# Performance work log

Hardware: AMD Instinct MI355X
Metric: run time of the kernel (lower is better)

## Reference

```python
import jax, jax.numpy as jnp
import numpy as np

B = 8192
D_LS, D_A, D_LM, D_AT, D_DS, D_DM = 1024, 512, 512, 512, 1024, 512
LENGTH = D_LS + D_A + D_LM  # 2048
OUT = 512


def setup_inputs() -> dict:
    key = jax.random.key(0)
    ks = jax.random.split(key, 9)
    return {
        "result_ls": jax.random.normal(ks[0], (B, 1, D_LS), jnp.float32),
        "result_A": jax.random.normal(ks[1], (B, 1, D_A), jnp.float32),
        "result_lm": jax.random.normal(ks[2], (B, 1, D_LM), jnp.float32),
        "result_AT": jax.random.normal(ks[3], (B, 1, D_AT), jnp.float32),
        "result_ds": jax.random.normal(ks[4], (B, 1, D_DS), jnp.float32),
        "result_dm": jax.random.normal(ks[5], (B, 1, D_DM), jnp.float32),
        "W": jax.random.normal(ks[6], (OUT, LENGTH), jnp.float32) * (1.0 / np.sqrt(LENGTH)),
        "b": jax.random.normal(ks[7], (OUT,), jnp.float32) * 0.01,
        "h_n": jax.random.normal(ks[8], (OUT, 1), jnp.float32) * (1.0 / np.sqrt(OUT)),
    }


def _pad_to(x, length):
    # zero-pad last dim of [B,1,d] to [B,1,length]
    return jnp.pad(x, ((0, 0), (0, 0), (0, length - x.shape[2])))


def reference(result_ls, result_A, result_lm, result_AT, result_ds, result_dm, W, b, h_n):
    # pad each node-type feature to common length and stack along node axis -> [B,6,L]
    nodes = jnp.concatenate(
        [_pad_to(t, LENGTH) for t in (result_ls, result_A, result_lm, result_AT, result_ds, result_dm)],
        axis=1,
    )
    temp = jnp.tanh(jnp.einsum("bnl,ol->bno", nodes, W) + b)  # [B,6,OUT]
    score = jnp.einsum("bno,oi->bni", temp, h_n)               # [B,6,1]
    score = score.reshape(-1, 1, 6)
    beta = jax.nn.softmax(score, axis=2)                        # [B,1,6]
    z_i = jnp.matmul(beta, nodes)                               # [B,1,L]
    return z_i
```

## Files before the change

kernel.cpp:

```cpp
#include <hip/hip_runtime.h>
#include <hip/hip_bf16.h>
#include <stdint.h>

typedef __attribute__((ext_vector_type(8))) short bf16x8;
typedef __attribute__((ext_vector_type(4))) float f32x4;

#define NB 8192

__device__ __forceinline__ unsigned pkbf(float x, float y) {
    __hip_bfloat162 h = __float22bfloat162_rn(make_float2(x, y));
    unsigned r;
    __builtin_memcpy(&r, &h, 4);
    return r;
}

__device__ __forceinline__ uint4 pack8(float4 a, float4 b) {
    uint4 r;
    r.x = pkbf(a.x, a.y);
    r.y = pkbf(a.z, a.w);
    r.z = pkbf(b.x, b.y);
    r.w = pkbf(b.z, b.w);
    return r;
}

__global__ __launch_bounds__(256)
void prep_w_kernel(const float* __restrict__ W, uint4* __restrict__ Wt) {
    int t = blockIdx.x * 256 + threadIdx.x;
    int lane = t & 63;
    int frag = t >> 6;
    int kb = frag >> 5, cb = frag & 31;
    int o = cb * 16 + (lane & 15);
    int k = kb * 32 + ((lane >> 4) << 3);
    const float* src = W + (size_t)o * 2048 + k;
    float4 a = *(const float4*)src;
    float4 b = *(const float4*)(src + 4);
    Wt[t] = pack8(a, b);
}

template<int MFN, int DN, int NN>
__global__ __launch_bounds__(512, 2)
void score_kernel(const float* __restrict__ p0, const float* __restrict__ p1,
                  const float* __restrict__ p2, const float* __restrict__ p3,
                  int n0, int n1, int n2, int n3,
                  const float* __restrict__ bias, const float* __restrict__ hvec,
                  const uint4* __restrict__ Wt, float* __restrict__ scores) {
    constexpr int BM = MFN * 16;
    constexpr int NST = DN / 64;
    constexpr int FRAGS = 2 * MFN;

    __shared__ uint4 lA[2][FRAGS * 64];
    __shared__ float red[8][BM];

    int bid = blockIdx.x;
    int ni = bid % NN;
    int tile = bid / NN;
    const float* xp; int node;
    switch (ni) {
        case 0: xp = p0; node = n0; break;
        case 1: xp = p1; node = n1; break;
        case 2: xp = p2; node = n2; break;
        default: xp = p3; node = n3; break;
    }
    int m0 = tile * BM;
    int t = threadIdx.x;
    int l = t & 63;
    int w = t >> 6;

    int cf = t >> 6;
    int r1 = (cf % MFN) * 16 + (l & 15);
    int k1 = (cf / MFN) * 32 + ((l >> 4) << 3);
    const float* g1 = xp + (size_t)(m0 + r1) * DN + k1;
    const float* g2 = g1 + 32;

    {
        float4 a0 = *(const float4*)g1;
        float4 a1 = *(const float4*)(g1 + 4);
        lA[0][t] = pack8(a0, a1);
        if constexpr (MFN == 8) {
            float4 b0 = *(const float4*)g2;
            float4 b1 = *(const float4*)(g2 + 4);
            lA[0][t + 512] = pack8(b0, b1);
        }
    }
    __syncthreads();

    f32x4 acc[MFN][4];
#pragma unroll
    for (int mf = 0; mf < MFN; ++mf)
#pragma unroll
        for (int nf = 0; nf < 4; ++nf)
            acc[mf][nf] = (f32x4){0.f, 0.f, 0.f, 0.f};

    for (int s = 0; s < NST; ++s) {
        int cur = s & 1;
        float4 a0, a1, b0, b1;
        bool hn = (s + 1) < NST;
        if (hn) {
            const float* q = g1 + (s + 1) * 64;
            a0 = *(const float4*)q;
            a1 = *(const float4*)(q + 4);
            if constexpr (MFN == 8) {
                const float* q2 = g2 + (s + 1) * 64;
                b0 = *(const float4*)q2;
                b1 = *(const float4*)(q2 + 4);
            }
        }
        bf16x8 bfr[2][4];
#pragma unroll
        for (int ks = 0; ks < 2; ++ks) {
            int kb = (s << 1) + ks;
            const uint4* wp = Wt + (((kb << 5) + (w << 2)) << 6) + l;
#pragma unroll
            for (int nf = 0; nf < 4; ++nf) {
                uint4 u = wp[nf << 6];
                __builtin_memcpy(&bfr[ks][nf], &u, 16);
            }
        }
#pragma unroll
        for (int ks = 0; ks < 2; ++ks) {
#pragma unroll
            for (int mf = 0; mf < MFN; ++mf) {
                uint4 u = lA[cur][(ks * MFN + mf) * 64 + l];
                bf16x8 afr;
                __builtin_memcpy(&afr, &u, 16);
#pragma unroll
                for (int nf = 0; nf < 4; ++nf)
                    acc[mf][nf] = __builtin_amdgcn_mfma_f32_16x16x32_bf16(
                        afr, bfr[ks][nf], acc[mf][nf], 0, 0, 0);
            }
        }
        if (hn) {
            lA[cur ^ 1][t] = pack8(a0, a1);
            if constexpr (MFN == 8)
                lA[cur ^ 1][t + 512] = pack8(b0, b1);
        }
        __syncthreads();
    }

    float bv[4], hv[4];
#pragma unroll
    for (int nf = 0; nf < 4; ++nf) {
        int o = (w << 6) + (nf << 4) + (l & 15);
        bv[nf] = bias[o];
        hv[nf] = hvec[o];
    }
#pragma unroll
    for (int mf = 0; mf < MFN; ++mf) {
        float sc[4] = {0.f, 0.f, 0.f, 0.f};
#pragma unroll
        for (int nf = 0; nf < 4; ++nf) {
#pragma unroll
            for (int r = 0; r < 4; ++r) {
                float xv = acc[mf][nf][r] + bv[nf];
                float th = 1.f - 2.f * __builtin_amdgcn_rcpf(1.f + __expf(2.f * xv));
                sc[r] = fmaf(hv[nf], th, sc[r]);
            }
        }
#pragma unroll
        for (int r = 0; r < 4; ++r) {
            float v = sc[r];
            v += __shfl_xor(v, 1);
            v += __shfl_xor(v, 2);
            v += __shfl_xor(v, 4);
            v += __shfl_xor(v, 8);
            if ((l & 15) == 0)
                red[w][(mf << 4) + ((l >> 4) << 2) + r] = v;
        }
    }
    __syncthreads();
    if (t < BM) {
        float ssum = 0.f;
#pragma unroll
        for (int w2 = 0; w2 < 8; ++w2) ssum += red[w2][t];
        scores[node * NB + m0 + t] = ssum;
    }
}

__global__ __launch_bounds__(256)
void z_kernel(const float* __restrict__ x0, const float* __restrict__ x1,
              const float* __restrict__ x2, const float* __restrict__ x3,
              const float* __restrict__ x4, const float* __restrict__ x5,
              const float* __restrict__ scores, float* __restrict__ out) {
    int wv = threadIdx.x >> 6;
    int lane = threadIdx.x & 63;
    int b = (blockIdx.x << 2) + wv;

    float s0 = scores[b];
    float s1 = scores[NB + b];
    float s2 = scores[2 * NB + b];
    float s3 = scores[3 * NB + b];
    float s4 = scores[4 * NB + b];
    float s5 = scores[5 * NB + b];
    float m = fmaxf(fmaxf(fmaxf(s0, s1), fmaxf(s2, s3)), fmaxf(s4, s5));
    float e0 = __expf(s0 - m), e1 = __expf(s1 - m), e2 = __expf(s2 - m);
    float e3 = __expf(s3 - m), e4 = __expf(s4 - m), e5 = __expf(s5 - m);
    float inv = __builtin_amdgcn_rcpf(e0 + e1 + e2 + e3 + e4 + e5);
    float b0 = e0 * inv, b1 = e1 * inv, b2 = e2 * inv;
    float b3 = e3 * inv, b4 = e4 * inv, b5 = e5 * inv;

    const float* pls = x0 + (size_t)b * 1024;
    const float* pA  = x1 + (size_t)b * 512;
    const float* plm = x2 + (size_t)b * 512;
    const float* pAT = x3 + (size_t)b * 512;
    const float* pds = x4 + (size_t)b * 1024;
    const float* pdm = x5 + (size_t)b * 512;
    float* po = out + (size_t)b * 2048;

#pragma unroll
    for (int j = 0; j < 2; ++j) {
        int c = (j << 8) + (lane << 2);
        float4 vls = *(const float4*)(pls + c);
        float4 vA  = *(const float4*)(pA + c);
        float4 vlm = *(const float4*)(plm + c);
        float4 vAT = *(const float4*)(pAT + c);
        float4 vds = *(const float4*)(pds + c);
        float4 vdm = *(const float4*)(pdm + c);
        float4 r;
        r.x = b0*vls.x + b1*vA.x + b2*vlm.x + b3*vAT.x + b4*vds.x + b5*vdm.x;
        r.y = b0*vls.y + b1*vA.y + b2*vlm.y + b3*vAT.y + b4*vds.y + b5*vdm.y;
        r.z = b0*vls.z + b1*vA.z + b2*vlm.z + b3*vAT.z + b4*vds.z + b5*vdm.z;
        r.w = b0*vls.w + b1*vA.w + b2*vlm.w + b3*vAT.w + b4*vds.w + b5*vdm.w;
        *(float4*)(po + c) = r;
    }
#pragma unroll
    for (int j = 0; j < 2; ++j) {
        int c = 512 + (j << 8) + (lane << 2);
        float4 vls = *(const float4*)(pls + c);
        float4 vds = *(const float4*)(pds + c);
        float4 r;
        r.x = b0*vls.x + b4*vds.x;
        r.y = b0*vls.y + b4*vds.y;
        r.z = b0*vls.z + b4*vds.z;
        r.w = b0*vls.w + b4*vds.w;
        *(float4*)(po + c) = r;
    }
    float4 zz = make_float4(0.f, 0.f, 0.f, 0.f);
#pragma unroll
    for (int j = 0; j < 4; ++j) {
        int c = 1024 + (j << 8) + (lane << 2);
        *(float4*)(po + c) = zz;
    }
}

extern "C" void kernel_launch(void* const* d_in, const int* in_sizes, int n_in,
                              void* d_out, int out_size, void* d_ws, size_t ws_size,
                              hipStream_t stream) {
    const float* x0   = (const float*)d_in[0];
    const float* x1   = (const float*)d_in[1];
    const float* x2   = (const float*)d_in[2];
    const float* x3   = (const float*)d_in[3];
    const float* x4   = (const float*)d_in[4];
    const float* x5   = (const float*)d_in[5];
    const float* W    = (const float*)d_in[6];
    const float* bias = (const float*)d_in[7];
    const float* hvec = (const float*)d_in[8];

    uint4* Wt = (uint4*)d_ws;
    float* scores = (float*)((char*)d_ws + (1u << 20));

    prep_w_kernel<<<256, 256, 0, stream>>>(W, Wt);
    score_kernel<4, 1024, 2><<<256, 512, 0, stream>>>(
        x0, x4, x0, x4, 0, 4, 0, 4, bias, hvec, Wt, scores);
    score_kernel<8, 512, 4><<<256, 512, 0, stream>>>(
        x1, x2, x3, x5, 1, 2, 3, 5, bias, hvec, Wt, scores);
    z_kernel<<<2048, 256, 0, stream>>>(x0, x1, x2, x3, x4, x5, scores, (float*)d_out);
}
```

Baseline: 101.5 us.

## Merge score kernels and preload full A tile into shared memory

The two score kernel launches become one launch of 512 blocks that branches on block index between the wide-feature and narrow-feature node paths. Each block now loads its whole activation tile (converted to bf16) into 128 KB of shared memory up front, instead of double-buffering 64-column slices with a barrier every step. The W fragments are software-prefetched one k-block ahead in registers. This removes a launch and the per-step barriers, but the large shared allocation limits occupancy to one block per CU and moves all global load latency ahead of the MFMA loop.

Result: faster. 94.36 us (-7.1%).

```diff
diff --git a/kernel.cpp b/kernel.cpp
--- a/kernel.cpp
+++ b/kernel.cpp
@@ -37,50 +37,28 @@
     Wt[t] = pack8(a, b);
 }
 
-template<int MFN, int DN, int NN>
-__global__ __launch_bounds__(512, 2)
-void score_kernel(const float* __restrict__ p0, const float* __restrict__ p1,
-                  const float* __restrict__ p2, const float* __restrict__ p3,
-                  int n0, int n1, int n2, int n3,
-                  const float* __restrict__ bias, const float* __restrict__ hvec,
-                  const uint4* __restrict__ Wt, float* __restrict__ scores) {
+template<int MFN, int DN>
+__device__ __forceinline__ void score_body(
+        const float* __restrict__ xp, int node, int m0,
+        const float* __restrict__ bias, const float* __restrict__ hvec,
+        const uint4* __restrict__ Wt, float* __restrict__ scores,
+        uint4* lA, float* red) {
     constexpr int BM = MFN * 16;
-    constexpr int NST = DN / 64;
-    constexpr int FRAGS = 2 * MFN;
-
-    __shared__ uint4 lA[2][FRAGS * 64];
-    __shared__ float red[8][BM];
-
-    int bid = blockIdx.x;
-    int ni = bid % NN;
-    int tile = bid / NN;
-    const float* xp; int node;
-    switch (ni) {
-        case 0: xp = p0; node = n0; break;
-        case 1: xp = p1; node = n1; break;
-        case 2: xp = p2; node = n2; break;
-        default: xp = p3; node = n3; break;
-    }
-    int m0 = tile * BM;
+    constexpr int NKB = DN / 32;
     int t = threadIdx.x;
     int l = t & 63;
     int w = t >> 6;
 
-    int cf = t >> 6;
-    int r1 = (cf % MFN) * 16 + (l & 15);
-    int k1 = (cf / MFN) * 32 + ((l >> 4) << 3);
-    const float* g1 = xp + (size_t)(m0 + r1) * DN + k1;
-    const float* g2 = g1 + 32;
-
-    {
-        float4 a0 = *(const float4*)g1;
-        float4 a1 = *(const float4*)(g1 + 4);
-        lA[0][t] = pack8(a0, a1);
-        if constexpr (MFN == 8) {
-            float4 b0 = *(const float4*)g2;
-            float4 b1 = *(const float4*)(g2 + 4);
-            lA[0][t + 512] = pack8(b0, b1);
-        }
+#pragma unroll
+    for (int j = 0; j < 16; ++j) {
+        int f = (t >> 6) + j * 8;
+        int kb = f / MFN, mf = f % MFN;
+        int row = mf * 16 + (l & 15);
+        int k = kb * 32 + ((l >> 4) << 3);
+        const float* g = xp + (size_t)(m0 + row) * DN + k;
+        float4 a = *(const float4*)g;
+        float4 b = *(const float4*)(g + 4);
+        lA[f * 64 + l] = pack8(a, b);
     }
     __syncthreads();
 
@@ -91,50 +69,37 @@
         for (int nf = 0; nf < 4; ++nf)
             acc[mf][nf] = (f32x4){0.f, 0.f, 0.f, 0.f};
 
-    for (int s = 0; s < NST; ++s) {
-        int cur = s & 1;
-        float4 a0, a1, b0, b1;
-        bool hn = (s + 1) < NST;
-        if (hn) {
-            const float* q = g1 + (s + 1) * 64;
-            a0 = *(const float4*)q;
-            a1 = *(const float4*)(q + 4);
-            if constexpr (MFN == 8) {
-                const float* q2 = g2 + (s + 1) * 64;
-                b0 = *(const float4*)q2;
-                b1 = *(const float4*)(q2 + 4);
-            }
-        }
-        bf16x8 bfr[2][4];
-#pragma unroll
-        for (int ks = 0; ks < 2; ++ks) {
-            int kb = (s << 1) + ks;
-            const uint4* wp = Wt + (((kb << 5) + (w << 2)) << 6) + l;
+    bf16x8 bcur[4];
+    {
+        const uint4* wp = Wt + ((0 + (w << 2)) << 6) + l;
+#pragma unroll
+        for (int nf = 0; nf < 4; ++nf) {
+            uint4 u = wp[nf << 6];
+            __builtin_memcpy(&bcur[nf], &u, 16);
+        }
+    }
+    for (int kb = 0; kb < NKB; ++kb) {
+        bf16x8 bnxt[4];
+        if (kb + 1 < NKB) {
+            const uint4* wp = Wt + ((((kb + 1) << 5) + (w << 2)) << 6) + l;
 #pragma unroll
             for (int nf = 0; nf < 4; ++nf) {
                 uint4 u = wp[nf << 6];
-                __builtin_memcpy(&bfr[ks][nf], &u, 16);
+                __builtin_memcpy(&bnxt[nf], &u, 16);
             }
         }
 #pragma unroll
-        for (int ks = 0; ks < 2; ++ks) {
-#pragma unroll
-            for (int mf = 0; mf < MFN; ++mf) {
-                uint4 u = lA[cur][(ks * MFN + mf) * 64 + l];
-                bf16x8 afr;
-                __builtin_memcpy(&afr, &u, 16);
-#pragma unroll
-                for (int nf = 0; nf < 4; ++nf)
-                    acc[mf][nf] = __builtin_amdgcn_mfma_f32_16x16x32_bf16(
-                        afr, bfr[ks][nf], acc[mf][nf], 0, 0, 0);
-            }
-        }
-        if (hn) {
-            lA[cur ^ 1][t] = pack8(a0, a1);
-            if constexpr (MFN == 8)
-                lA[cur ^ 1][t + 512] = pack8(b0, b1);
-        }
-        __syncthreads();
+        for (int mf = 0; mf < MFN; ++mf) {
+            uint4 u = lA[(kb * MFN + mf) * 64 + l];
+            bf16x8 afr;
+            __builtin_memcpy(&afr, &u, 16);
+#pragma unroll
+            for (int nf = 0; nf < 4; ++nf)
+                acc[mf][nf] = __builtin_amdgcn_mfma_f32_16x16x32_bf16(
+                    afr, bcur[nf], acc[mf][nf], 0, 0, 0);
+        }
+#pragma unroll
+        for (int nf = 0; nf < 4; ++nf) bcur[nf] = bnxt[nf];
     }
 
     float bv[4], hv[4];
@@ -164,15 +129,40 @@
             v += __shfl_xor(v, 4);
             v += __shfl_xor(v, 8);
             if ((l & 15) == 0)
-                red[w][(mf << 4) + ((l >> 4) << 2) + r] = v;
+                red[w * BM + (mf << 4) + ((l >> 4) << 2) + r] = v;
         }
     }
     __syncthreads();
     if (t < BM) {
         float ssum = 0.f;
 #pragma unroll
-        for (int w2 = 0; w2 < 8; ++w2) ssum += red[w2][t];
+        for (int w2 = 0; w2 < 8; ++w2) ssum += red[w2 * BM + t];
         scores[node * NB + m0 + t] = ssum;
+    }
+}
+
+__global__ __launch_bounds__(512, 2)
+void score_kernel(const float* __restrict__ x0, const float* __restrict__ x1,
+                  const float* __restrict__ x2, const float* __restrict__ x3,
+                  const float* __restrict__ x4, const float* __restrict__ x5,
+                  const float* __restrict__ bias, const float* __restrict__ hvec,
+                  const uint4* __restrict__ Wt, float* __restrict__ scores) {
+    __shared__ uint4 lA[8192];
+    __shared__ float red[8 * 128];
+
+    int bid = blockIdx.x;
+    if (bid < 256) {
+        const float* xp = (bid & 1) ? x4 : x0;
+        int node = (bid & 1) ? 4 : 0;
+        int m0 = (bid >> 1) * 64;
+        score_body<4, 1024>(xp, node, m0, bias, hvec, Wt, scores, lA, red);
+    } else {
+        int lb = bid - 256;
+        int ni = lb & 3;
+        const float* xp = (ni == 0) ? x1 : (ni == 1) ? x2 : (ni == 2) ? x3 : x5;
+        int node = (ni == 0) ? 1 : (ni == 1) ? 2 : (ni == 2) ? 3 : 5;
+        int m0 = (lb >> 2) * 128;
+        score_body<8, 512>(xp, node, m0, bias, hvec, Wt, scores, lA, red);
     }
 }
 
@@ -259,9 +249,6 @@
     float* scores = (float*)((char*)d_ws + (1u << 20));
 
     prep_w_kernel<<<256, 256, 0, stream>>>(W, Wt);
-    score_kernel<4, 1024, 2><<<256, 512, 0, stream>>>(
-        x0, x4, x0, x4, 0, 4, 0, 4, bias, hvec, Wt, scores);
-    score_kernel<8, 512, 4><<<256, 512, 0, stream>>>(
-        x1, x2, x3, x5, 1, 2, 3, 5, bias, hvec, Wt, scores);
+    score_kernel<<<512, 512, 0, stream>>>(x0, x1, x2, x3, x4, x5, bias, hvec, Wt, scores);
     z_kernel<<<2048, 256, 0, stream>>>(x0, x1, x2, x3, x4, x5, scores, (float*)d_out);
 }
```
